# Kernel tuning notes

Measured on AMD Instinct MI355X. Metric: run time of the kernel, lower is better.

Reference implementation:

```python
import jax, jax.numpy as jnp
import numpy as np

H, D, R, S, K, EV = 8, 256, 6, 2, 2, 2   # num_heads, head_dim, ratio, shared_head, topk, expand_v
HID = 2048
DV = D * EV            # head_v_dim = 512
KEY_DIM = H * D        # 2048
VAL_DIM = KEY_DIM * EV # 4096


def setup_inputs() -> dict:
    key = jax.random.key(0)
    ks = jax.random.split(key, 9)
    b, t = 2, 1024
    def lin(k, fan_in, shape):
        # ~torch default linear init scale
        return jax.random.normal(k, shape, jnp.float32) * (fan_in ** -0.5)
    return {
        "hidden_states": jax.random.normal(ks[0], (b, t, HID), jnp.float32),
        "Wq": lin(ks[1], HID, (HID, KEY_DIM)),
        "Wk": lin(ks[2], HID, (HID, KEY_DIM)),
        "Wv": lin(ks[3], HID, (HID, VAL_DIM)),
        "Wq_exp": lin(ks[4], D, (H, D, D * R)),  # per-head q expert expansion (ModuleList -> batched)
        "Wk_exp": lin(ks[5], D, (H, D, D * R)),
        "Wgate": lin(ks[6], D, (D, R - S)),
        "Wg": lin(ks[7], HID, (HID, VAL_DIM)),
        "Wo": lin(ks[8], VAL_DIM, (VAL_DIM, HID)),
    }


def reference(hidden_states, Wq, Wk, Wv, Wq_exp, Wk_exp, Wgate, Wg, Wo):
    b, t, _ = hidden_states.shape
    # base projections, split into heads: [H, b, t, D]
    q = (hidden_states @ Wq).reshape(b, t, H, D).transpose(2, 0, 1, 3)
    k = (hidden_states @ Wk).reshape(b, t, H, D).transpose(2, 0, 1, 3)
    v = (hidden_states @ Wv).reshape(b, t, H, DV)  # [b, t, H, DV]

    # --- sparse routing on q (gate over ratio - shared experts) ---
    logits = jnp.einsum('hbtd,dn->hbtn', q, Wgate)
    scores = jax.nn.softmax(logits.astype(jnp.float32), axis=-1)
    w, idx = jax.lax.top_k(scores, K)
    w = w / jnp.sum(w, axis=-1, keepdims=True)
    idx = idx + S  # shift past shared experts
    # scatter top-k weights into full [H, b, t, R]
    full = jnp.sum(jax.nn.one_hot(idx, R, dtype=w.dtype) * w[..., None], axis=-2)
    full = full.at[..., :S].set(1.0 / S)
    full = full / jnp.sum(full, axis=-1, keepdims=True)
    rw = full.astype(hidden_states.dtype).transpose(3, 1, 2, 0)  # [R, b, t, H]
    mask = (rw != 0).astype(hidden_states.dtype)                 # [R, b, t, H]

    # --- per-head expert expansions: [R, b, t, H, D] ---
    qe = jnp.einsum('hbtd,hde->hbte', q, Wq_exp).reshape(H, b, t, R, D).transpose(3, 1, 2, 0, 4)
    ke = jnp.einsum('hbtd,hde->hbte', k, Wk_exp).reshape(H, b, t, R, D).transpose(3, 1, 2, 0, 4)
    ve = jnp.broadcast_to(v[None], (R, b, t, H, DV))
    qe = qe * mask[..., None]
    ke = ke * mask[..., None]
    ve = ve * mask[..., None]

    # --- dense attention per (expert, batch, head) ---
    attn = jax.nn.softmax(jnp.einsum('rbqhd,rbkhd->rbhqk', qe, ke) / (D ** 0.5), axis=-1)
    o = jnp.einsum('rbhqk,rbkhd->rbqhd', attn, ve)  # [R, b, t, H, DV]

    # --- weighted combine over experts + gated output ---
    o = jnp.einsum('rbthd,rbth->bthd', o, rw)
    g = (hidden_states @ Wg).reshape(b, t, H, DV)
    o = o * jax.nn.silu(g)
    return o.reshape(b, t, VAL_DIM) @ Wo
```

## Files before the change

### kernel.cpp

```cpp
#include <hip/hip_runtime.h>
#include <hip/hip_bf16.h>
#include <cstdint>
#include <cstddef>

typedef __bf16 bf16_t;
typedef __bf16 bf16x8 __attribute__((ext_vector_type(8)));
typedef float f32x4 __attribute__((ext_vector_type(4)));

typedef __attribute__((address_space(3))) unsigned int lds_uint_t;
typedef __attribute__((address_space(1))) unsigned int glob_uint_t;

__device__ __forceinline__ void gload16(const void* g, void* l) {
  __builtin_amdgcn_global_load_lds((const glob_uint_t*)g, (lds_uint_t*)l, 16, 0, 0);
}

__device__ __forceinline__ f32x4 mfma16(bf16x8 a, bf16x8 b, f32x4 c) {
  return __builtin_amdgcn_mfma_f32_16x16x32_bf16(a, b, c, 0, 0, 0);
}

__global__ __launch_bounds__(256) void conv_bf16_k(const float* __restrict__ in,
                                                   bf16_t* __restrict__ out, int n8) {
  int i = blockIdx.x * 256 + threadIdx.x;
  if (i >= n8) return;
  f32x4 a = *(const f32x4*)(in + (size_t)i * 8);
  f32x4 b = *(const f32x4*)(in + (size_t)i * 8 + 4);
  bf16x8 o;
  o[0] = (bf16_t)a[0]; o[1] = (bf16_t)a[1]; o[2] = (bf16_t)a[2]; o[3] = (bf16_t)a[3];
  o[4] = (bf16_t)b[0]; o[5] = (bf16_t)b[1]; o[6] = (bf16_t)b[2]; o[7] = (bf16_t)b[3];
  *(bf16x8*)(out + (size_t)i * 8) = o;
}

__global__ __launch_bounds__(256) void tconv_k(const float* __restrict__ in, bf16_t* __restrict__ out,
                                               int R, int C, size_t inZ, size_t outZ) {
  __shared__ __align__(16) bf16_t t[64 * 72];
  in += (size_t)blockIdx.z * inZ;
  out += (size_t)blockIdx.z * outZ;
  const int c0 = blockIdx.x * 64, r0 = blockIdx.y * 64;
  const int tid = threadIdx.x;
#pragma unroll
  for (int it = 0; it < 4; it++) {
    int c = tid + it * 256;
    int row = c >> 4, ch = c & 15;
    f32x4 v = *(const f32x4*)(in + (size_t)(r0 + row) * C + c0 + ch * 4);
#pragma unroll
    for (int j = 0; j < 4; j++) t[(ch * 4 + j) * 72 + row] = (bf16_t)v[j];
  }
  __syncthreads();
#pragma unroll
  for (int it = 0; it < 2; it++) {
    int c = tid + it * 256;
    int oc = c >> 3, ch = c & 7;
    bf16x8 v = *(const bf16x8*)(t + oc * 72 + ch * 8);
    *(bf16x8*)(out + (size_t)(c0 + oc) * R + r0 + ch * 8) = v;
  }
}

__global__ __launch_bounds__(256) void tv_k(const bf16_t* __restrict__ v, bf16_t* __restrict__ Vt) {
  __shared__ __align__(16) bf16_t t[64 * 72];
  const int tt0 = blockIdx.x * 64;
  const int dv0 = blockIdx.y * 64;
  const int bh = blockIdx.z;
  const int b = bh >> 3, h = bh & 7;
  const int tid = threadIdx.x;
  const bf16_t* src = v + (size_t)(b * 1024 + tt0) * 12288 + 8192 + h * 512 + dv0;
#pragma unroll
  for (int it = 0; it < 2; it++) {
    int c = tid + it * 256;
    int row = c >> 3, ch = c & 7;
    bf16x8 x = *(const bf16x8*)(src + (size_t)row * 12288 + ch * 8);
#pragma unroll
    for (int j = 0; j < 8; j++) t[(ch * 8 + j) * 72 + row] = x[j];
  }
  __syncthreads();
  bf16_t* dst = Vt + (size_t)bh * 524288 + (size_t)dv0 * 1024 + tt0;
#pragma unroll
  for (int it = 0; it < 2; it++) {
    int c = tid + it * 256;
    int od = c >> 3, ch = c & 7;
    bf16x8 x = *(const bf16x8*)(t + od * 72 + ch * 8);
    *(bf16x8*)(dst + (size_t)od * 1024 + ch * 8) = x;
  }
}

__global__ __launch_bounds__(256) void wfuse_k(const float* __restrict__ Wq, const float* __restrict__ Wgate,
                                               float* __restrict__ Wf) {
  __shared__ float wg[1024];
  const int tid = threadIdx.x;
  for (int i = tid; i < 1024; i += 256) wg[i] = Wgate[i];
  __syncthreads();
  const int kk = blockIdx.x * 64 + (tid & 63);
  const int oid = tid >> 6;
  float acc[8] = {0, 0, 0, 0, 0, 0, 0, 0};
  const float* wr = Wq + (size_t)kk * 2048;
#pragma unroll
  for (int half = 0; half < 2; half++) {
    const int h = oid * 2 + half;
    const float* seg = wr + h * 256;
    for (int d = 0; d < 256; d += 4) {
      f32x4 q4 = *(const f32x4*)(seg + d);
#pragma unroll
      for (int n = 0; n < 4; n++) {
        acc[half * 4 + n] += q4[0] * wg[(d + 0) * 4 + n] + q4[1] * wg[(d + 1) * 4 + n] +
                             q4[2] * wg[(d + 2) * 4 + n] + q4[3] * wg[(d + 3) * 4 + n];
      }
    }
  }
#pragma unroll
  for (int jj = 0; jj < 8; jj++) Wf[(size_t)kk * 32 + oid * 8 + jj] = acc[jj];
}

__global__ __launch_bounds__(256) void logits_k(const float* __restrict__ hs, const float* __restrict__ Wf,
                                                float* __restrict__ lg) {
  __shared__ __align__(16) float hrow[2048];
  __shared__ float red[8][32];
  const int bt = blockIdx.x;
  const int tid = threadIdx.x;
  const float* src = hs + (size_t)bt * 2048;
  for (int i = tid; i < 512; i += 256) *(f32x4*)&hrow[i * 4] = *(const f32x4*)(src + i * 4);
  __syncthreads();
  const int j = tid & 31, part = tid >> 5;
  float acc = 0.f;
  for (int kk = part * 256; kk < part * 256 + 256; kk++) acc += hrow[kk] * Wf[(size_t)kk * 32 + j];
  red[part][j] = acc;
  __syncthreads();
  if (tid < 32) {
    float s = 0.f;
#pragma unroll
    for (int p = 0; p < 8; p++) s += red[p][tid];
    lg[(size_t)bt * 32 + tid] = s;
  }
}

__global__ __launch_bounds__(256) void routing_k(const float* __restrict__ lg, float* __restrict__ rw) {
  int gid = blockIdx.x * 256 + threadIdx.x;
  if (gid >= 16384) return;
  const int h = gid >> 11;
  const int bt = gid & 2047;
  const int b = bt >> 10, tt = bt & 1023;
  f32x4 l = *(const f32x4*)(lg + (size_t)bt * 32 + h * 4);
  float mx = fmaxf(fmaxf(l[0], l[1]), fmaxf(l[2], l[3]));
  float e0 = __expf(l[0] - mx), e1 = __expf(l[1] - mx), e2 = __expf(l[2] - mx), e3 = __expf(l[3] - mx);
  float den = e0 + e1 + e2 + e3;
  float s[4] = {e0 / den, e1 / den, e2 / den, e3 / den};
  int i1 = 0;
#pragma unroll
  for (int i = 1; i < 4; i++) if (s[i] > s[i1]) i1 = i;
  int i2 = (i1 == 0) ? 1 : 0;
#pragma unroll
  for (int i = 0; i < 4; i++) if (i != i1 && s[i] > s[i2]) i2 = i;
  float sw = s[i1] + s[i2];
  float w1 = s[i1] / sw, w2 = s[i2] / sw;
  float tot = 1.0f + w1 + w2;
  float o[6] = {0.5f / tot, 0.5f / tot, 0.f, 0.f, 0.f, 0.f};
  o[2 + i1] = w1 / tot;
  o[2 + i2] = w2 / tot;
#pragma unroll
  for (int r = 0; r < 6; r++) rw[(size_t)((r * 2 + b) * 8 + h) * 1024 + tt] = o[r];
}

template <int MODE>
__global__ __launch_bounds__(256) void gemm_bt(const bf16_t* __restrict__ A, const bf16_t* __restrict__ B,
                                               void* __restrict__ Cp, int K, int lda, int ldb, int ldc) {
  __shared__ __align__(16) bf16_t lsA[128 * 64];
  __shared__ __align__(16) bf16_t lsB[128 * 64];
  const int tid = threadIdx.x;
  const int lane = tid & 63, wv = tid >> 6;
  const int lrow = lane & 15, lgrp = lane >> 4;
  const int wr = wv >> 1, wc = wv & 1;
  const int bn = blockIdx.x * 128, bm = blockIdx.y * 128;

  f32x4 zero = {0.f, 0.f, 0.f, 0.f};
  f32x4 acc[4][4];
#pragma unroll
  for (int i = 0; i < 4; i++)
#pragma unroll
    for (int j = 0; j < 4; j++) acc[i][j] = zero;

  for (int k0 = 0; k0 < K; k0 += 64) {
    __syncthreads();
#pragma unroll
    for (int it = 0; it < 4; it++) {
      int c = tid + it * 256;
      int row = c >> 3, coff = (c & 7) * 16;
      gload16((const char*)A + ((size_t)(bm + row) * lda + k0) * 2 + coff, (char*)lsA + row * 128 + coff);
      gload16((const char*)B + ((size_t)(bn + row) * ldb + k0) * 2 + coff, (char*)lsB + row * 128 + coff);
    }
    __syncthreads();
#pragma unroll
    for (int kk = 0; kk < 2; kk++) {
      bf16x8 af[4], bfr[4];
#pragma unroll
      for (int m4 = 0; m4 < 4; m4++)
        af[m4] = *(const bf16x8*)((const char*)lsA + (wr * 64 + m4 * 16 + lrow) * 128 + kk * 64 + lgrp * 16);
#pragma unroll
      for (int n4 = 0; n4 < 4; n4++)
        bfr[n4] = *(const bf16x8*)((const char*)lsB + (wc * 64 + n4 * 16 + lrow) * 128 + kk * 64 + lgrp * 16);
#pragma unroll
      for (int m4 = 0; m4 < 4; m4++)
#pragma unroll
        for (int n4 = 0; n4 < 4; n4++) acc[m4][n4] = mfma16(af[m4], bfr[n4], acc[m4][n4]);
    }
  }
#pragma unroll
  for (int m4 = 0; m4 < 4; m4++) {
#pragma unroll
    for (int i = 0; i < 4; i++) {
      const int row = bm + wr * 64 + m4 * 16 + lgrp * 4 + i;
#pragma unroll
      for (int n4 = 0; n4 < 4; n4++) {
        const int col = bn + wc * 64 + n4 * 16 + lrow;
        float v = acc[m4][n4][i];
        if constexpr (MODE == 0) {
          ((bf16_t*)Cp)[(size_t)row * ldc + col] = (bf16_t)v;
        } else {
          ((float*)Cp)[(size_t)row * ldc + col] = v;
        }
      }
    }
  }
}

__global__ __launch_bounds__(256) void gemm_n64(const bf16_t* __restrict__ A, const bf16_t* __restrict__ B,
                                                float* __restrict__ C, int K, int lda, int ldb, int ldc) {
  __shared__ __align__(16) bf16_t lsA[128 * 64];
  __shared__ __align__(16) bf16_t lsB[64 * 64];
  const int tid = threadIdx.x;
  const int lane = tid & 63, wr = tid >> 6;
  const int lrow = lane & 15, lgrp = lane >> 4;
  const int bn = blockIdx.x * 64, bm = blockIdx.y * 128;

  f32x4 zero = {0.f, 0.f, 0.f, 0.f};
  f32x4 acc[2][4];
#pragma unroll
  for (int i = 0; i < 2; i++)
#pragma unroll
    for (int j = 0; j < 4; j++) acc[i][j] = zero;

  for (int k0 = 0; k0 < K; k0 += 64) {
    __syncthreads();
#pragma unroll
    for (int it = 0; it < 4; it++) {
      int c = tid + it * 256;
      int row = c >> 3, coff = (c & 7) * 16;
      gload16((const char*)A + ((size_t)(bm + row) * lda + k0) * 2 + coff, (char*)lsA + row * 128 + coff);
    }
#pragma unroll
    for (int it = 0; it < 2; it++) {
      int c = tid + it * 256;
      int row = c >> 3, coff = (c & 7) * 16;
      gload16((const char*)B + ((size_t)(bn + row) * ldb + k0) * 2 + coff, (char*)lsB + row * 128 + coff);
    }
    __syncthreads();
#pragma unroll
    for (int kk = 0; kk < 2; kk++) {
      bf16x8 af[2], bfr[4];
#pragma unroll
      for (int m2 = 0; m2 < 2; m2++)
        af[m2] = *(const bf16x8*)((const char*)lsA + (wr * 32 + m2 * 16 + lrow) * 128 + kk * 64 + lgrp * 16);
#pragma unroll
      for (int n4 = 0; n4 < 4; n4++)
        bfr[n4] = *(const bf16x8*)((const char*)lsB + (n4 * 16 + lrow) * 128 + kk * 64 + lgrp * 16);
#pragma unroll
      for (int m2 = 0; m2 < 2; m2++)
#pragma unroll
        for (int n4 = 0; n4 < 4; n4++) acc[m2][n4] = mfma16(af[m2], bfr[n4], acc[m2][n4]);
    }
  }
#pragma unroll
  for (int m2 = 0; m2 < 2; m2++) {
#pragma unroll
    for (int i = 0; i < 4; i++) {
      const int row = bm + wr * 32 + m2 * 16 + lgrp * 4 + i;
#pragma unroll
      for (int n4 = 0; n4 < 4; n4++) {
        C[(size_t)row * ldc + bn + n4 * 16 + lrow] = acc[m2][n4][i];
      }
    }
  }
}

__global__ __launch_bounds__(256) void gemm_exp(const bf16_t* __restrict__ qkg, const bf16_t* __restrict__ Wqe,
                                                const bf16_t* __restrict__ Wke, bf16_t* __restrict__ qeB,
                                                bf16_t* __restrict__ keB) {
  __shared__ __align__(16) bf16_t lsA[128 * 64];
  __shared__ __align__(16) bf16_t lsB[128 * 64];
  const int tid = threadIdx.x;
  const int lane = tid & 63, wv = tid >> 6;
  const int lrow = lane & 15, lgrp = lane >> 4;
  const int wr = wv >> 1, wc = wv & 1;
  const int bn = blockIdx.x * 128, bm = blockIdx.y * 128;
  const int z = blockIdx.z;
  const int sel = z >> 3, hh = z & 7;
  const bf16_t* A = qkg + sel * 2048 + hh * 256;
  const bf16_t* B = (sel ? Wke : Wqe) + (size_t)hh * 393216;
  bf16_t* C = sel ? keB : qeB;

  f32x4 zero = {0.f, 0.f, 0.f, 0.f};
  f32x4 acc[4][4];
#pragma unroll
  for (int i = 0; i < 4; i++)
#pragma unroll
    for (int j = 0; j < 4; j++) acc[i][j] = zero;

  for (int k0 = 0; k0 < 256; k0 += 64) {
    __syncthreads();
#pragma unroll
    for (int it = 0; it < 4; it++) {
      int c = tid + it * 256;
      int row = c >> 3, coff = (c & 7) * 16;
      gload16((const char*)A + ((size_t)(bm + row) * 12288 + k0) * 2 + coff, (char*)lsA + row * 128 + coff);
      gload16((const char*)B + ((size_t)(bn + row) * 256 + k0) * 2 + coff, (char*)lsB + row * 128 + coff);
    }
    __syncthreads();
#pragma unroll
    for (int kk = 0; kk < 2; kk++) {
      bf16x8 af[4], bfr[4];
#pragma unroll
      for (int m4 = 0; m4 < 4; m4++)
        af[m4] = *(const bf16x8*)((const char*)lsA + (wr * 64 + m4 * 16 + lrow) * 128 + kk * 64 + lgrp * 16);
#pragma unroll
      for (int n4 = 0; n4 < 4; n4++)
        bfr[n4] = *(const bf16x8*)((const char*)lsB + (wc * 64 + n4 * 16 + lrow) * 128 + kk * 64 + lgrp * 16);
#pragma unroll
      for (int m4 = 0; m4 < 4; m4++)
#pragma unroll
        for (int n4 = 0; n4 < 4; n4++) acc[m4][n4] = mfma16(af[m4], bfr[n4], acc[m4][n4]);
    }
  }
#pragma unroll
  for (int m4 = 0; m4 < 4; m4++) {
#pragma unroll
    for (int i = 0; i < 4; i++) {
      const int row = bm + wr * 64 + m4 * 16 + lgrp * 4 + i;
      const int bb = row >> 10, tt = row & 1023;
#pragma unroll
      for (int n4 = 0; n4 < 4; n4++) {
        const int col = bn + wc * 64 + n4 * 16 + lrow;
        const int rr = col >> 8, dd = col & 255;
        C[((size_t)((rr * 2 + bb) * 8 + hh) * 1024 + tt) * 256 + dd] = (bf16_t)acc[m4][n4][i];
      }
    }
  }
}

__global__ __launch_bounds__(128, 2) void attn_k(const bf16_t* __restrict__ qe, const bf16_t* __restrict__ ke,
                                                 const bf16_t* __restrict__ Vt, const float* __restrict__ rw,
                                                 const bf16_t* __restrict__ g, bf16_t* __restrict__ oc) {
  __shared__ __align__(16) bf16_t ldsK[32 * 256];
  __shared__ __align__(16) bf16_t ldsV[256 * 32];
  __shared__ __align__(16) bf16_t ldsP[2 * 16 * 40];

  const int f = (blockIdx.x & 7) * 128 + (blockIdx.x >> 3);
  const int dvh = f & 1, qt = (f >> 1) & 31, bh = f >> 6;

  const int tid = threadIdx.x;
  const int wv = tid >> 6, lane = tid & 63;
  const int lrow = lane & 15, lgrp = lane >> 4;
  const int b = bh >> 3, h = bh & 7;
  const int qw = qt * 32 + wv * 16;

  const char* vbase = (const char*)Vt + ((size_t)bh * 524288 + (size_t)dvh * 262144) * 2;

  auto issue_tile = [&](int rr, int kt) {
    const char* kb = (const char*)ke + ((size_t)((rr * 2 + b) * 8 + h) * 262144 + (size_t)kt * 8192) * 2;
    char* lk = (char*)ldsK;
#pragma unroll
    for (int it = 0; it < 8; it++) {
      int p = it * 2048 + tid * 16;
      int row = p >> 9, off = p & 511;
      gload16(kb + (size_t)row * 512 + (off ^ ((row & 7) << 4)), lk + p);
    }
    const char* vb = vbase + kt * 64;
    char* lv = (char*)ldsV;
#pragma unroll
    for (int it = 0; it < 8; it++) {
      int p = it * 2048 + tid * 16;
      int row = p >> 6, off = p & 63;
      gload16(vb + (size_t)row * 2048 + (off ^ (((row >> 1) & 3) << 4)), lv + p);
    }
  };

  f32x4 zero = {0.f, 0.f, 0.f, 0.f};
  f32x4 Otot[16];
#pragma unroll
  for (int n = 0; n < 16; n++) Otot[n] = zero;

  for (int r = 0; r < 6; r++) {
    const size_t rbh = (size_t)((r * 2 + b) * 8 + h);
    const bf16_t* qbase = qe + rbh * 262144;
    const float* rwb = rw + rbh * 1024;

    bf16x8 qf[8];
#pragma unroll
    for (int c = 0; c < 8; c++)
      qf[c] = *(const bf16x8*)(qbase + (size_t)(qw + lrow) * 256 + c * 32 + lgrp * 8);
    float rwq[4];
#pragma unroll
    for (int i = 0; i < 4; i++) rwq[i] = rwb[qw + lgrp * 4 + i];

    float Lp[4] = {0.f, 0.f, 0.f, 0.f};
    f32x4 accO[16];
#pragma unroll
    for (int n = 0; n < 16; n++) accO[n] = zero;

    for (int kt = 0; kt < 32; kt++) {
      issue_tile(r, kt);
      asm volatile("s_waitcnt vmcnt(0) lgkmcnt(0)" ::: "memory");
      __syncthreads();

      const char* lK = (const char*)ldsK;
      const char* lV = (const char*)ldsV;
      const float* rwk = rwb + kt * 32;
      float mk0 = rwk[lrow], mk1 = rwk[16 + lrow];

      f32x4 sac0 = zero, sac1 = zero;
      __builtin_amdgcn_s_setprio(1);
#pragma unroll
      for (int c = 0; c < 8; c++) {
        int col = (c * 64 + lgrp * 16) ^ ((lrow & 7) << 4);
        bf16x8 k0 = *(const bf16x8*)(lK + (size_t)lrow * 512 + col);
        bf16x8 k1 = *(const bf16x8*)(lK + (size_t)(16 + lrow) * 512 + col);
        sac0 = mfma16(qf[c], k0, sac0);
        sac1 = mfma16(qf[c], k1, sac1);
      }
      __builtin_amdgcn_s_setprio(0);
      bf16_t* pb = ldsP + wv * 640;
#pragma unroll
      for (int i = 0; i < 4; i++) {
        float e0 = __expf(sac0[i] * 0.0625f);
        float e1 = __expf(sac1[i] * 0.0625f);
        pb[(i * 4 + lgrp) * 40 + lrow] = (bf16_t)((mk0 != 0.f) ? e0 : 0.f);
        pb[(i * 4 + lgrp) * 40 + 16 + lrow] = (bf16_t)((mk1 != 0.f) ? e1 : 0.f);
        Lp[i] += ((mk0 != 0.f) ? e0 : 1.f) + ((mk1 != 0.f) ? e1 : 1.f);
      }
      bf16x8 pa = *(const bf16x8*)(pb + ((lrow & 3) * 4 + (lrow >> 2)) * 40 + lgrp * 8);
      __builtin_amdgcn_s_setprio(1);
#pragma unroll
      for (int n = 0; n < 16; n++) {
        int row = n * 16 + lrow;
        int col = (lgrp * 16) ^ (((row >> 1) & 3) << 4);
        bf16x8 vf = *(const bf16x8*)(lV + (size_t)row * 64 + col);
        accO[n] = mfma16(pa, vf, accO[n]);
      }
      __builtin_amdgcn_s_setprio(0);
      __syncthreads();
    }
#pragma unroll
    for (int i = 0; i < 4; i++) {
      float v = Lp[i];
      v += __shfl_xor(v, 1, 16);
      v += __shfl_xor(v, 2, 16);
      v += __shfl_xor(v, 4, 16);
      v += __shfl_xor(v, 8, 16);
      float inv = rwq[i] / v;
#pragma unroll
      for (int n = 0; n < 16; n++) Otot[n][i] += accO[n][i] * inv;
    }
  }

#pragma unroll
  for (int i = 0; i < 4; i++) {
    const size_t grow = ((size_t)(b * 1024 + qw + lgrp * 4 + i)) * 12288 + 4096 + h * 512 + dvh * 256;
    const size_t orow = ((size_t)(b * 1024 + qw + lgrp * 4 + i)) * 4096 + h * 512 + dvh * 256;
#pragma unroll
    for (int n = 0; n < 16; n++) {
      float gv = (float)g[grow + n * 16 + lrow];
      float sg = gv / (1.f + __expf(-gv));
      oc[orow + n * 16 + lrow] = (bf16_t)(Otot[n][i] * sg);
    }
  }
}

extern "C" void kernel_launch(void* const* d_in, const int* in_sizes, int n_in,
                              void* d_out, int out_size, void* d_ws, size_t ws_size,
                              hipStream_t stream) {
  const float* hs  = (const float*)d_in[0];
  const float* Wq  = (const float*)d_in[1];
  const float* Wk  = (const float*)d_in[2];
  const float* Wv  = (const float*)d_in[3];
  const float* Wqe = (const float*)d_in[4];
  const float* Wke = (const float*)d_in[5];
  const float* Wgt = (const float*)d_in[6];
  const float* Wg  = (const float*)d_in[7];
  const float* Wo  = (const float*)d_in[8];
  float* out = (float*)d_out;

  const size_t MB = 1024 * 1024;
  char* w = (char*)d_ws;
  bf16_t* hs_bf = (bf16_t*)(w + 0 * MB);
  bf16_t* WcatT = (bf16_t*)(w + 8 * MB);
  bf16_t* qeB   = (bf16_t*)(w + 0 * MB);
  bf16_t* WoT   = (bf16_t*)(w + 56 * MB);
  bf16_t* WqeT  = (bf16_t*)(w + 72 * MB);
  bf16_t* WkeT  = (bf16_t*)(w + 78 * MB);
  bf16_t* qkg   = (bf16_t*)(w + 84 * MB);
  bf16_t* Vt    = (bf16_t*)(w + 132 * MB);
  bf16_t* keB   = (bf16_t*)(w + 148 * MB);
  bf16_t* ocB   = (bf16_t*)(w + 196 * MB);
  float*  Wf    = (float*)(w + 212 * MB);
  float*  lg    = (float*)(w + 212 * MB + 262144);
  float*  rwB   = (float*)(w + 212 * MB + 524288);
  (void)ws_size; (void)in_sizes; (void)n_in; (void)out_size;

  conv_bf16_k<<<2048, 256, 0, stream>>>(hs, hs_bf, 524288);
  tconv_k<<<dim3(32, 32, 1), 256, 0, stream>>>(Wq, WcatT, 2048, 2048, 0, 0);
  tconv_k<<<dim3(32, 32, 1), 256, 0, stream>>>(Wk, WcatT + 2048 * 2048, 2048, 2048, 0, 0);
  tconv_k<<<dim3(64, 32, 1), 256, 0, stream>>>(Wg, WcatT + 4096 * 2048, 2048, 4096, 0, 0);
  tconv_k<<<dim3(64, 32, 1), 256, 0, stream>>>(Wv, WcatT + 8192 * 2048, 2048, 4096, 0, 0);
  tconv_k<<<dim3(32, 64, 1), 256, 0, stream>>>(Wo, WoT, 4096, 2048, 0, 0);
  tconv_k<<<dim3(24, 4, 8), 256, 0, stream>>>(Wqe, WqeT, 256, 1536, 393216, 393216);
  tconv_k<<<dim3(24, 4, 8), 256, 0, stream>>>(Wke, WkeT, 256, 1536, 393216, 393216);

  wfuse_k<<<32, 256, 0, stream>>>(Wq, Wgt, Wf);
  logits_k<<<2048, 256, 0, stream>>>(hs, Wf, lg);
  routing_k<<<64, 256, 0, stream>>>(lg, rwB);

  gemm_bt<0><<<dim3(96, 16, 1), 256, 0, stream>>>(hs_bf, WcatT, qkg, 2048, 2048, 2048, 12288);
  tv_k<<<dim3(16, 8, 16), 256, 0, stream>>>(qkg, Vt);

  gemm_exp<<<dim3(12, 16, 16), 256, 0, stream>>>(qkg, WqeT, WkeT, qeB, keB);

  attn_k<<<1024, 128, 0, stream>>>(qeB, keB, Vt, rwB, qkg, ocB);

  gemm_n64<<<dim3(32, 16, 1), 256, 0, stream>>>(ocB, WoT, out, 4096, 4096, 4096, 2048);
}
```

Measured before the change: 763.0 us.

## Restructure attention kernel with 32x32 MFMA, larger query tiles, double-buffered K/V

Rewrites the attention kernel so each block has 4 waves covering 128 queries and a quarter of the value dimension, using 32x32x16 MFMA instead of 16x16x32. K/V tiles are double-buffered in LDS, so the next tile's global-to-LDS load is issued before computing on the current one, and the trailing barrier is dropped. Each K tile is now shared by more queries, cutting repeated K loads, while V work per block shrinks. The cost is more LDS per block and higher register pressure from 16-wide accumulators.

```diff
diff --git a/kernel.cpp b/kernel.cpp
--- a/kernel.cpp
+++ b/kernel.cpp
@@ -6,6 +6,7 @@
 typedef __bf16 bf16_t;
 typedef __bf16 bf16x8 __attribute__((ext_vector_type(8)));
 typedef float f32x4 __attribute__((ext_vector_type(4)));
+typedef float f32x16 __attribute__((ext_vector_type(16)));
 
 typedef __attribute__((address_space(3))) unsigned int lds_uint_t;
 typedef __attribute__((address_space(1))) unsigned int glob_uint_t;
@@ -16,6 +17,9 @@
 
 __device__ __forceinline__ f32x4 mfma16(bf16x8 a, bf16x8 b, f32x4 c) {
   return __builtin_amdgcn_mfma_f32_16x16x32_bf16(a, b, c, 0, 0, 0);
+}
+__device__ __forceinline__ f32x16 mfma32(bf16x8 a, bf16x8 b, f32x16 c) {
+  return __builtin_amdgcn_mfma_f32_32x32x16_bf16(a, b, c, 0, 0, 0);
 }
 
 __global__ __launch_bounds__(256) void conv_bf16_k(const float* __restrict__ in,
@@ -343,130 +347,147 @@
   }
 }
 
-__global__ __launch_bounds__(128, 2) void attn_k(const bf16_t* __restrict__ qe, const bf16_t* __restrict__ ke,
+__global__ __launch_bounds__(256, 2) void attn_k(const bf16_t* __restrict__ qe, const bf16_t* __restrict__ ke,
                                                  const bf16_t* __restrict__ Vt, const float* __restrict__ rw,
                                                  const bf16_t* __restrict__ g, bf16_t* __restrict__ oc) {
-  __shared__ __align__(16) bf16_t ldsK[32 * 256];
-  __shared__ __align__(16) bf16_t ldsV[256 * 32];
-  __shared__ __align__(16) bf16_t ldsP[2 * 16 * 40];
-
-  const int f = (blockIdx.x & 7) * 128 + (blockIdx.x >> 3);
-  const int dvh = f & 1, qt = (f >> 1) & 31, bh = f >> 6;
+  __shared__ __align__(16) bf16_t ldsK[2][32 * 256];
+  __shared__ __align__(16) bf16_t ldsV[2][128 * 32];
+  __shared__ __align__(16) bf16_t ldsP[4][32 * 32];
+
+  const int f = (blockIdx.x & 7) * 64 + (blockIdx.x >> 3);
+  const int dvq = f & 3, qt = (f >> 2) & 7, bh = f >> 5;
 
   const int tid = threadIdx.x;
   const int wv = tid >> 6, lane = tid & 63;
-  const int lrow = lane & 15, lgrp = lane >> 4;
+  const int kq = lane & 31, hi = lane >> 5;
   const int b = bh >> 3, h = bh & 7;
-  const int qw = qt * 32 + wv * 16;
-
-  const char* vbase = (const char*)Vt + ((size_t)bh * 524288 + (size_t)dvh * 262144) * 2;
-
-  auto issue_tile = [&](int rr, int kt) {
+  const int qw = qt * 128 + wv * 32;
+
+  const char* vbase = (const char*)Vt + ((size_t)bh * 524288 + (size_t)dvq * 131072) * 2;
+
+  auto issue_tile = [&](int rr, int kt, int buf) {
     const char* kb = (const char*)ke + ((size_t)((rr * 2 + b) * 8 + h) * 262144 + (size_t)kt * 8192) * 2;
-    char* lk = (char*)ldsK;
-#pragma unroll
-    for (int it = 0; it < 8; it++) {
-      int p = it * 2048 + tid * 16;
+    char* lk = (char*)ldsK[buf];
+#pragma unroll
+    for (int it = 0; it < 4; it++) {
+      int p = (wv * 4 + it) * 1024 + (lane << 4);
       int row = p >> 9, off = p & 511;
       gload16(kb + (size_t)row * 512 + (off ^ ((row & 7) << 4)), lk + p);
     }
     const char* vb = vbase + kt * 64;
-    char* lv = (char*)ldsV;
-#pragma unroll
-    for (int it = 0; it < 8; it++) {
-      int p = it * 2048 + tid * 16;
+    char* lv = (char*)ldsV[buf];
+#pragma unroll
+    for (int it = 0; it < 2; it++) {
+      int p = (wv * 2 + it) * 1024 + (lane << 4);
       int row = p >> 6, off = p & 63;
       gload16(vb + (size_t)row * 2048 + (off ^ (((row >> 1) & 3) << 4)), lv + p);
     }
   };
 
-  f32x4 zero = {0.f, 0.f, 0.f, 0.f};
-  f32x4 Otot[16];
-#pragma unroll
-  for (int n = 0; n < 16; n++) Otot[n] = zero;
+  f32x16 zero16 = {0.f};
+  f32x16 Otot[4];
+#pragma unroll
+  for (int n = 0; n < 4; n++) Otot[n] = zero16;
+
+  char* pw = (char*)ldsP[wv];
+  const int vr = (kq & 3) ^ ((kq >> 2) & 3);
+
+  int cur = 0;
+  issue_tile(0, 0, 0);
 
   for (int r = 0; r < 6; r++) {
     const size_t rbh = (size_t)((r * 2 + b) * 8 + h);
     const bf16_t* qbase = qe + rbh * 262144;
     const float* rwb = rw + rbh * 1024;
 
-    bf16x8 qf[8];
-#pragma unroll
-    for (int c = 0; c < 8; c++)
-      qf[c] = *(const bf16x8*)(qbase + (size_t)(qw + lrow) * 256 + c * 32 + lgrp * 8);
-    float rwq[4];
-#pragma unroll
-    for (int i = 0; i < 4; i++) rwq[i] = rwb[qw + lgrp * 4 + i];
-
-    float Lp[4] = {0.f, 0.f, 0.f, 0.f};
-    f32x4 accO[16];
-#pragma unroll
-    for (int n = 0; n < 16; n++) accO[n] = zero;
+    bf16x8 qf[16];
+    {
+      const bf16_t* qrow = qbase + (size_t)(qw + kq) * 256 + hi * 8;
+#pragma unroll
+      for (int s = 0; s < 16; s++) qf[s] = *(const bf16x8*)(qrow + s * 16);
+    }
+
+    float Lp[16];
+#pragma unroll
+    for (int rg = 0; rg < 16; rg++) Lp[rg] = 0.f;
+    f32x16 accO[4];
+#pragma unroll
+    for (int n = 0; n < 4; n++) accO[n] = zero16;
 
     for (int kt = 0; kt < 32; kt++) {
-      issue_tile(r, kt);
       asm volatile("s_waitcnt vmcnt(0) lgkmcnt(0)" ::: "memory");
       __syncthreads();
-
-      const char* lK = (const char*)ldsK;
-      const char* lV = (const char*)ldsV;
-      const float* rwk = rwb + kt * 32;
-      float mk0 = rwk[lrow], mk1 = rwk[16 + lrow];
-
-      f32x4 sac0 = zero, sac1 = zero;
+      {
+        int nr = r + ((kt == 31) ? 1 : 0);
+        int nkt = (kt + 1) & 31;
+        if (nr < 6) issue_tile(nr, nkt, cur ^ 1);
+      }
+      const char* lK = (const char*)ldsK[cur];
+      const char* lV = (const char*)ldsV[cur];
+      const float mk = rwb[kt * 32 + kq];
+
+      f32x16 sA = zero16, sB = zero16;
       __builtin_amdgcn_s_setprio(1);
 #pragma unroll
-      for (int c = 0; c < 8; c++) {
-        int col = (c * 64 + lgrp * 16) ^ ((lrow & 7) << 4);
-        bf16x8 k0 = *(const bf16x8*)(lK + (size_t)lrow * 512 + col);
-        bf16x8 k1 = *(const bf16x8*)(lK + (size_t)(16 + lrow) * 512 + col);
-        sac0 = mfma16(qf[c], k0, sac0);
-        sac1 = mfma16(qf[c], k1, sac1);
+      for (int s = 0; s < 16; s += 2) {
+        bf16x8 k0 = *(const bf16x8*)(lK + (size_t)kq * 512 + ((s * 32 + hi * 16) ^ ((kq & 7) << 4)));
+        bf16x8 k1 = *(const bf16x8*)(lK + (size_t)kq * 512 + (((s + 1) * 32 + hi * 16) ^ ((kq & 7) << 4)));
+        sA = mfma32(qf[s], k0, sA);
+        sB = mfma32(qf[s + 1], k1, sB);
       }
       __builtin_amdgcn_s_setprio(0);
-      bf16_t* pb = ldsP + wv * 640;
-#pragma unroll
-      for (int i = 0; i < 4; i++) {
-        float e0 = __expf(sac0[i] * 0.0625f);
-        float e1 = __expf(sac1[i] * 0.0625f);
-        pb[(i * 4 + lgrp) * 40 + lrow] = (bf16_t)((mk0 != 0.f) ? e0 : 0.f);
-        pb[(i * 4 + lgrp) * 40 + 16 + lrow] = (bf16_t)((mk1 != 0.f) ? e1 : 0.f);
-        Lp[i] += ((mk0 != 0.f) ? e0 : 1.f) + ((mk1 != 0.f) ? e1 : 1.f);
-      }
-      bf16x8 pa = *(const bf16x8*)(pb + ((lrow & 3) * 4 + (lrow >> 2)) * 40 + lgrp * 8);
+
+      const bool act = (mk != 0.f);
+#pragma unroll
+      for (int rg = 0; rg < 16; rg++) {
+        float e = __expf((sA[rg] + sB[rg]) * 0.0625f);
+        Lp[rg] += act ? e : 1.f;
+        const int q32 = (rg & 3) + 8 * (rg >> 2) + 4 * hi;
+        const int vq = (rg & 3) ^ ((2 * (rg >> 2) + hi) & 3);
+        *(bf16_t*)(pw + q32 * 64 + ((kq * 2) ^ (vq << 4))) = (bf16_t)(act ? e : 0.f);
+      }
+
+      bf16x8 pa0 = *(const bf16x8*)(pw + kq * 64 + ((hi * 16) ^ (vr << 4)));
+      bf16x8 pa1 = *(const bf16x8*)(pw + kq * 64 + ((32 + hi * 16) ^ (vr << 4)));
       __builtin_amdgcn_s_setprio(1);
 #pragma unroll
-      for (int n = 0; n < 16; n++) {
-        int row = n * 16 + lrow;
-        int col = (lgrp * 16) ^ (((row >> 1) & 3) << 4);
-        bf16x8 vf = *(const bf16x8*)(lV + (size_t)row * 64 + col);
-        accO[n] = mfma16(pa, vf, accO[n]);
+      for (int n = 0; n < 4; n++) {
+        const size_t vrow = (size_t)(n * 32 + kq) * 64;
+        const int vswz = ((kq >> 1) & 3) << 4;
+        bf16x8 v0 = *(const bf16x8*)(lV + vrow + ((hi * 16) ^ vswz));
+        bf16x8 v1 = *(const bf16x8*)(lV + vrow + ((32 + hi * 16) ^ vswz));
+        accO[n] = mfma32(pa0, v0, accO[n]);
+        accO[n] = mfma32(pa1, v1, accO[n]);
       }
       __builtin_amdgcn_s_setprio(0);
-      __syncthreads();
-    }
-#pragma unroll
-    for (int i = 0; i < 4; i++) {
-      float v = Lp[i];
-      v += __shfl_xor(v, 1, 16);
-      v += __shfl_xor(v, 2, 16);
-      v += __shfl_xor(v, 4, 16);
-      v += __shfl_xor(v, 8, 16);
-      float inv = rwq[i] / v;
-#pragma unroll
-      for (int n = 0; n < 16; n++) Otot[n][i] += accO[n][i] * inv;
-    }
-  }
-
-#pragma unroll
-  for (int i = 0; i < 4; i++) {
-    const size_t grow = ((size_t)(b * 1024 + qw + lgrp * 4 + i)) * 12288 + 4096 + h * 512 + dvh * 256;
-    const size_t orow = ((size_t)(b * 1024 + qw + lgrp * 4 + i)) * 4096 + h * 512 + dvh * 256;
-#pragma unroll
-    for (int n = 0; n < 16; n++) {
-      float gv = (float)g[grow + n * 16 + lrow];
+      cur ^= 1;
+    }
+
+#pragma unroll
+    for (int rg = 0; rg < 16; rg++) {
+      float v = Lp[rg];
+      v += __shfl_xor(v, 1, 32);
+      v += __shfl_xor(v, 2, 32);
+      v += __shfl_xor(v, 4, 32);
+      v += __shfl_xor(v, 8, 32);
+      v += __shfl_xor(v, 16, 32);
+      const int q32 = (rg & 3) + 8 * (rg >> 2) + 4 * hi;
+      float wq = rwb[qw + q32] / v;
+#pragma unroll
+      for (int n = 0; n < 4; n++) Otot[n][rg] += accO[n][rg] * wq;
+    }
+  }
+
+#pragma unroll
+  for (int rg = 0; rg < 16; rg++) {
+    const int q32 = (rg & 3) + 8 * (rg >> 2) + 4 * hi;
+    const size_t grow = ((size_t)(b * 1024 + qw + q32)) * 12288 + 4096 + h * 512 + dvq * 128 + kq;
+    const size_t orow = ((size_t)(b * 1024 + qw + q32)) * 4096 + h * 512 + dvq * 128 + kq;
+#pragma unroll
+    for (int n = 0; n < 4; n++) {
+      float gv = (float)g[grow + n * 32];
       float sg = gv / (1.f + __expf(-gv));
-      oc[orow + n * 16 + lrow] = (bf16_t)(Otot[n][i] * sg);
+      oc[orow + n * 32] = (bf16_t)(Otot[n][rg] * sg);
     }
   }
 }
@@ -520,7 +541,7 @@
 
   gemm_exp<<<dim3(12, 16, 16), 256, 0, stream>>>(qkg, WqeT, WkeT, qeB, keB);
 
-  attn_k<<<1024, 128, 0, stream>>>(qeB, keB, Vt, rwB, qkg, ocB);
+  attn_k<<<512, 256, 0, stream>>>(qeB, keB, Vt, rwB, qkg, ocB);
 
   gemm_n64<<<dim3(32, 16, 1), 256, 0, stream>>>(ocB, WoT, out, 4096, 4096, 4096, 2048);
 }
```

Measured after the change: 837.6 us. +9.8%, slower.

## Double-buffer K/V tiles in attention and widen blocks to four waves

Applied to the files above, without the earlier changes.

The attention kernel now double-buffers the K and V LDS tiles, prefetching the next tile (crossing expert boundaries) right after the barrier so global loads overlap the MFMA work, and it drops the trailing barrier. Blocks grow from 2 to 4 waves (64 query rows), which halves the grid and lets more waves share each loaded K/V tile. The cost is doubled LDS per block, which may limit occupancy. A single barrier per iteration combined with a prefetch into the other buffer is enough to keep the pipeline race-free.

```diff
diff --git a/kernel.cpp b/kernel.cpp
--- a/kernel.cpp
+++ b/kernel.cpp
@@ -343,38 +343,38 @@
   }
 }
 
-__global__ __launch_bounds__(128, 2) void attn_k(const bf16_t* __restrict__ qe, const bf16_t* __restrict__ ke,
+__global__ __launch_bounds__(256, 2) void attn_k(const bf16_t* __restrict__ qe, const bf16_t* __restrict__ ke,
                                                  const bf16_t* __restrict__ Vt, const float* __restrict__ rw,
                                                  const bf16_t* __restrict__ g, bf16_t* __restrict__ oc) {
-  __shared__ __align__(16) bf16_t ldsK[32 * 256];
-  __shared__ __align__(16) bf16_t ldsV[256 * 32];
-  __shared__ __align__(16) bf16_t ldsP[2 * 16 * 40];
-
-  const int f = (blockIdx.x & 7) * 128 + (blockIdx.x >> 3);
-  const int dvh = f & 1, qt = (f >> 1) & 31, bh = f >> 6;
+  __shared__ __align__(16) bf16_t ldsK[2][32 * 256];
+  __shared__ __align__(16) bf16_t ldsV[2][256 * 32];
+  __shared__ __align__(16) bf16_t ldsP[4 * 16 * 40];
+
+  const int f = (blockIdx.x & 7) * 64 + (blockIdx.x >> 3);
+  const int qt = f & 15, dvh = (f >> 4) & 1, bh = f >> 5;
 
   const int tid = threadIdx.x;
   const int wv = tid >> 6, lane = tid & 63;
   const int lrow = lane & 15, lgrp = lane >> 4;
   const int b = bh >> 3, h = bh & 7;
-  const int qw = qt * 32 + wv * 16;
+  const int qw = qt * 64 + wv * 16;
 
   const char* vbase = (const char*)Vt + ((size_t)bh * 524288 + (size_t)dvh * 262144) * 2;
 
-  auto issue_tile = [&](int rr, int kt) {
+  auto issue_tile = [&](int rr, int kt, int buf) {
     const char* kb = (const char*)ke + ((size_t)((rr * 2 + b) * 8 + h) * 262144 + (size_t)kt * 8192) * 2;
-    char* lk = (char*)ldsK;
-#pragma unroll
-    for (int it = 0; it < 8; it++) {
-      int p = it * 2048 + tid * 16;
+    char* lk = (char*)ldsK[buf];
+#pragma unroll
+    for (int it = 0; it < 4; it++) {
+      int p = (wv * 4 + it) * 1024 + (lane << 4);
       int row = p >> 9, off = p & 511;
       gload16(kb + (size_t)row * 512 + (off ^ ((row & 7) << 4)), lk + p);
     }
     const char* vb = vbase + kt * 64;
-    char* lv = (char*)ldsV;
-#pragma unroll
-    for (int it = 0; it < 8; it++) {
-      int p = it * 2048 + tid * 16;
+    char* lv = (char*)ldsV[buf];
+#pragma unroll
+    for (int it = 0; it < 4; it++) {
+      int p = (wv * 4 + it) * 1024 + (lane << 4);
       int row = p >> 6, off = p & 63;
       gload16(vb + (size_t)row * 2048 + (off ^ (((row >> 1) & 3) << 4)), lv + p);
     }
@@ -384,6 +384,9 @@
   f32x4 Otot[16];
 #pragma unroll
   for (int n = 0; n < 16; n++) Otot[n] = zero;
+
+  int cur = 0;
+  issue_tile(0, 0, 0);
 
   for (int r = 0; r < 6; r++) {
     const size_t rbh = (size_t)((r * 2 + b) * 8 + h);
@@ -404,12 +407,15 @@
     for (int n = 0; n < 16; n++) accO[n] = zero;
 
     for (int kt = 0; kt < 32; kt++) {
-      issue_tile(r, kt);
       asm volatile("s_waitcnt vmcnt(0) lgkmcnt(0)" ::: "memory");
       __syncthreads();
-
-      const char* lK = (const char*)ldsK;
-      const char* lV = (const char*)ldsV;
+      {
+        int nr = r + ((kt == 31) ? 1 : 0);
+        int nkt = (kt + 1) & 31;
+        if (nr < 6) issue_tile(nr, nkt, cur ^ 1);
+      }
+      const char* lK = (const char*)ldsK[cur];
+      const char* lV = (const char*)ldsV[cur];
       const float* rwk = rwb + kt * 32;
       float mk0 = rwk[lrow], mk1 = rwk[16 + lrow];
 
@@ -443,7 +449,7 @@
         accO[n] = mfma16(pa, vf, accO[n]);
       }
       __builtin_amdgcn_s_setprio(0);
-      __syncthreads();
+      cur ^= 1;
     }
 #pragma unroll
     for (int i = 0; i < 4; i++) {
@@ -520,7 +526,7 @@
 
   gemm_exp<<<dim3(12, 16, 16), 256, 0, stream>>>(qkg, WqeT, WkeT, qeB, keB);
 
-  attn_k<<<1024, 128, 0, stream>>>(qeB, keB, Vt, rwB, qkg, ocB);
+  attn_k<<<512, 256, 0, stream>>>(qeB, keB, Vt, rwB, qkg, ocB);
 
   gemm_n64<<<dim3(32, 16, 1), 256, 0, stream>>>(ocB, WoT, out, 4096, 4096, 4096, 2048);
 }
```

After: 701.0 us. 1.09x faster.
